# Kernel tuning notes

Hardware: AMD Instinct MI355X
Metric: run time of the kernel (lower is better)

The kernel has to match this reference:

```python
import jax, jax.numpy as jnp
import numpy as np

VOCAB = 5000
EMB = 128
H1 = 128
H2 = 64
Q = 64
T = 256
B = 512
LTEXT = 30
EOS = 2  # padding_idx row of the embedding is zero


def setup_inputs() -> dict:
    rng = jax.random.key(0)
    ks = jax.random.split(rng, 16)
    f = lambda k, s: jax.random.normal(k, s, dtype=jnp.float32) * 0.05
    emb = f(ks[0], (VOCAB, EMB)).at[EOS].set(0.0)
    return {
        "key": jax.random.normal(ks[1], (T, B, Q), dtype=jnp.float32),
        "values": jax.random.normal(ks[2], (T, B, Q), dtype=jnp.float32),
        "mask": jnp.ones((B, 1, T), dtype=jnp.float32),
        "text": jax.random.randint(ks[3], (B, LTEXT), 0, VOCAB),
        "emb": emb,
        "W_ih1": f(ks[4], (4 * H1, EMB + Q)), "W_hh1": f(ks[5], (4 * H1, H1)),
        "b_ih1": f(ks[6], (4 * H1,)), "b_hh1": f(ks[7], (4 * H1,)),
        "W_ih2": f(ks[8], (4 * H2, H1)), "W_hh2": f(ks[9], (4 * H2, H2)),
        "b_ih2": f(ks[10], (4 * H2,)), "b_hh2": f(ks[11], (4 * H2,)),
        "W_q": f(ks[12], (Q, H2)), "b_q": f(ks[13], (Q,)),
        "W_out": f(ks[14], (VOCAB, H2 + Q)), "b_out": f(ks[15], (VOCAB,)),
    }


def _lstm_cell(x, h, c, Wih, Whh, bih, bhh):
    # torch.nn.LSTMCell: gates ordered (input, forget, cell, output)
    g = x @ Wih.T + bih + h @ Whh.T + bhh
    i, f, gg, o = jnp.split(g, 4, axis=-1)
    c2 = jax.nn.sigmoid(f) * c + jax.nn.sigmoid(i) * jnp.tanh(gg)
    h2 = jax.nn.sigmoid(o) * jnp.tanh(c2)
    return h2, c2


def reference(key, values, mask, text, emb,
              W_ih1, W_hh1, b_ih1, b_hh1,
              W_ih2, W_hh2, b_ih2, b_hh2,
              W_q, b_q, W_out, b_out):
    # isTrain=True, teacher_forcing_ratio=1.0, use_gumbel_noise=False:
    # every step uses the teacher-forced embedding embeddings[:, i, :].
    bsz = key.shape[1]
    L = text.shape[1] - 1
    h1d = W_hh1.shape[1]
    h2d = W_hh2.shape[1]
    qd = W_q.shape[0]
    xs = jnp.swapaxes(emb[text[:, :L]], 0, 1)          # (L, B, EMB)
    m = mask[:, 0, :]                                   # (B, T)

    def step(carry, x):
        h1, c1, h2, c2, ctx = carry
        inp = jnp.concatenate([x, ctx], axis=1)         # (B, EMB+Q)
        h1, c1 = _lstm_cell(inp, h1, c1, W_ih1, W_hh1, b_ih1, b_hh1)
        h2, c2 = _lstm_cell(h1, h2, c2, W_ih2, W_hh2, b_ih2, b_hh2)
        q = h2 @ W_q.T + b_q                            # (B, Q)
        energy = jnp.einsum('bk,tbk->bt', q, key)       # (B, T)
        attn = jax.nn.softmax(energy, axis=-1)
        ma = m * attn
        ma = ma / jnp.maximum(jnp.sum(ma, axis=-1, keepdims=True), 2e-30)
        ctx = jnp.einsum('bt,tbv->bv', ma, values)      # (B, Q)
        pred = jnp.concatenate([h2, ctx], axis=1) @ W_out.T + b_out  # (B, V)
        return (h1, c1, h2, c2, ctx), pred

    z = lambda d: jnp.zeros((bsz, d), dtype=jnp.float32)
    carry0 = (z(h1d), z(h1d), z(h2d), z(h2d), z(qd))
    _, preds = jax.lax.scan(step, carry0, xs)           # (L, B, V)
    return jnp.swapaxes(preds, 0, 1)                    # (B, L, V)
```

## Files before the change

kernel.cpp:

```cpp
#include <hip/hip_runtime.h>
#include <hip/hip_bf16.h>
#include <hip/hip_fp16.h>

#define VOCAB 5000
#define EMB 128
#define H1D 128
#define H2D 64
#define QD 64
#define TDIM 256
#define BDIM 512
#define LTEXT 30
#define LSTEPS 29

typedef __attribute__((ext_vector_type(4))) float f32x4;
typedef __attribute__((ext_vector_type(8))) _Float16 f16x8;
typedef __attribute__((ext_vector_type(2))) _Float16 h2v;

#define OFF_WOUT  0u
#define OFF_W1H   0x140000u
#define OFF_W2H   (OFF_W1H + 512u*320u*2u)
#define OFF_WQH   (OFF_W2H + 256u*192u*2u)
#define OFF_B1    (OFF_WQH + 64u*64u*2u)
#define OFF_B2    (OFF_B1 + 512u*4u)
#define OFF_H2CTX 0x1B0000u

__device__ __forceinline__ float sigmoidf_(float x) {
    return 1.0f / (1.0f + __expf(-x));
}

__device__ __forceinline__ float dot8(f16x8 w, f16x8 u, float acc) {
    union U8 { f16x8 v; h2v h[4]; };
    U8 W; W.v = w; U8 X; X.v = u;
#if __has_builtin(__builtin_amdgcn_fdot2)
    acc = __builtin_amdgcn_fdot2(W.h[0], X.h[0], acc, false);
    acc = __builtin_amdgcn_fdot2(W.h[1], X.h[1], acc, false);
    acc = __builtin_amdgcn_fdot2(W.h[2], X.h[2], acc, false);
    acc = __builtin_amdgcn_fdot2(W.h[3], X.h[3], acc, false);
#else
    #pragma unroll
    for (int i = 0; i < 8; ++i) acc += (float)w[i] * (float)u[i];
#endif
    return acc;
}

__global__ void k_cvt_f16(const float* __restrict__ W, _Float16* __restrict__ Wh, int n) {
    int i = blockIdx.x * 256 + threadIdx.x;
    if (i < n) Wh[i] = (_Float16)W[i];
}

__global__ void k_prep_w1(const float* __restrict__ Wih1, const float* __restrict__ Whh1,
                          const float* __restrict__ bih1, const float* __restrict__ bhh1,
                          _Float16* __restrict__ W1h, float* __restrict__ bias1) {
    int g = blockIdx.x;
    int k = threadIdx.x;
    float v = (k < 192) ? Wih1[g * 192 + k] : Whh1[g * 128 + (k - 192)];
    W1h[g * 320 + k] = (_Float16)v;
    if (k == 0) bias1[g] = bih1[g] + bhh1[g];
}

__global__ void k_prep_w2(const float* __restrict__ Wih2, const float* __restrict__ Whh2,
                          const float* __restrict__ bih2, const float* __restrict__ bhh2,
                          _Float16* __restrict__ W2h, float* __restrict__ bias2) {
    int g = blockIdx.x;
    int k = threadIdx.x;
    float v = (k < 128) ? Wih2[g * 128 + k] : Whh2[g * 64 + (k - 128)];
    W2h[g * 192 + k] = (_Float16)v;
    if (k == 0) bias2[g] = bih2[g] + bhh2[g];
}

__global__ __launch_bounds__(512, 2) void k_recurrent(
    const float* __restrict__ key, const float* __restrict__ values,
    const float* __restrict__ mask, const int* __restrict__ text,
    const float* __restrict__ emb,
    const _Float16* __restrict__ W1h, const float* __restrict__ bias1,
    const _Float16* __restrict__ W2h, const float* __restrict__ bias2,
    const _Float16* __restrict__ Wqh, const float* __restrict__ bq,
    _Float16* __restrict__ h2ctx)
{
    __shared__ alignas(16) _Float16 s_key16[2 * 256 * 64];
    __shared__ alignas(16) _Float16 s_valT [2 * 64 * 256];
    __shared__ alignas(16) _Float16 s_x16[2][2][128];
    __shared__ alignas(16) _Float16 s_Wq[64 * 64];
    __shared__ alignas(16) _Float16 s_v16[2][192];
    __shared__ alignas(16) _Float16 s_ctx16[2][64];
    __shared__ alignas(16) _Float16 s_q16[2][64];
    __shared__ alignas(16) _Float16 s_ma16[2 * 256];
    __shared__ _Float16 s_mask16[2 * 256];
    __shared__ float s_g1[2][512];
    __shared__ float s_g2p[2][2][256];
    __shared__ float s_cp[2][4][64];
    __shared__ float s_redM[8], s_redA[8], s_redB[8];
    __shared__ int   s_tok[2][LSTEPS];

    const int tid = threadIdx.x;
    const int b0 = blockIdx.x * 2;

    f16x8 w1[40];
    {
        const f16x8* w1g = (const f16x8*)(W1h + (size_t)tid * 320);
        #pragma unroll
        for (int c = 0; c < 40; ++c) w1[c] = w1g[c];
    }
    const float bias1r = bias1[tid];
    const float bias2r = (tid < 256) ? bias2[tid] : 0.f;
    const float bqr    = (tid < 128) ? bq[tid & 63] : 0.f;

    if (tid < 64) {
        int r = tid >> 5, tt = tid & 31;
        if (tt < LSTEPS) s_tok[r][tt] = text[(b0 + r) * LTEXT + tt];
    }
    if (tid < 256) {
        int r = tid >> 7, k = tid & 127;
        int tok = text[(b0 + r) * LTEXT];
        s_x16[0][r][k] = (_Float16)emb[(size_t)tok * EMB + k];
    }
    {
        int qj = tid >> 3, c = tid & 7;
        f16x8 w = *(const f16x8*)(Wqh + (qj << 6) + (c << 3));
        *(f16x8*)&s_Wq[(qj << 6) + (((c ^ (qj & 7))) << 3)] = w;
    }
    {
        int r = tid >> 8, tk = tid & 255;
        s_mask16[tid] = (_Float16)mask[(size_t)(b0 + r) * TDIM + tk];
    }
    if (tid < 384) ((_Float16*)s_v16)[tid] = (_Float16)0.f;
    if (tid < 128) ((_Float16*)s_ctx16)[tid] = (_Float16)0.f;

    {
        const int tq  = tid >> 7;
        const int idx = tid & 127;
        const int r = idx >> 6, kk = idx & 63;
        #pragma unroll 4
        for (int it = 0; it < 64; ++it) {
            int t = (it << 2) + tq;
            size_t g = ((size_t)t * BDIM + b0 + r) * QD + kk;
            float kf = key[g];
            float vf = values[g];
            s_key16[(((r << 8) + t) << 6) + ((((kk >> 3) ^ (t & 7))) << 3) + (kk & 7)] = (_Float16)kf;
            s_valT [(((r << 6) + kk) << 8) + ((((t >> 3) ^ (kk & 31))) << 3) + (t & 7)] = (_Float16)vf;
        }
    }

    float c1reg = 0.f;
    float c2reg = 0.f;
    __syncthreads();

    #pragma unroll 1
    for (int t = 0; t < LSTEPS; ++t) {
        float xpref = 0.f;
        const int pr = tid >> 7, pk = tid & 127;
        const bool havepref = (t + 1 < LSTEPS) && (tid < 256);
        if (havepref) {
            int tok = s_tok[pr][t + 1];
            xpref = emb[(size_t)tok * EMB + pk];
        }

        {
            const f16x8* xc0 = (const f16x8*)&s_x16[t & 1][0][0];
            const f16x8* xc1 = (const f16x8*)&s_x16[t & 1][1][0];
            const f16x8* cc0 = (const f16x8*)&s_ctx16[0][0];
            const f16x8* cc1 = (const f16x8*)&s_ctx16[1][0];
            const f16x8* hh0 = (const f16x8*)&s_v16[0][0];
            const f16x8* hh1 = (const f16x8*)&s_v16[1][0];
            float a0 = bias1r, a1 = bias1r;
            #pragma unroll
            for (int c = 0; c < 16; ++c) { f16x8 w = w1[c];      a0 = dot8(w, xc0[c], a0); a1 = dot8(w, xc1[c], a1); }
            #pragma unroll
            for (int c = 0; c < 8;  ++c) { f16x8 w = w1[16 + c]; a0 = dot8(w, cc0[c], a0); a1 = dot8(w, cc1[c], a1); }
            #pragma unroll
            for (int c = 0; c < 16; ++c) { f16x8 w = w1[24 + c]; a0 = dot8(w, hh0[c], a0); a1 = dot8(w, hh1[c], a1); }
            s_g1[0][tid] = a0;
            s_g1[1][tid] = a1;
        }
        __syncthreads();

        if (tid < 256) {
            int r = tid >> 7, j = tid & 127;
            float gi = s_g1[r][j], gf = s_g1[r][128 + j];
            float gg = s_g1[r][256 + j], go = s_g1[r][384 + j];
            float c = sigmoidf_(gf) * c1reg + sigmoidf_(gi) * tanhf(gg);
            c1reg = c;
            float h = sigmoidf_(go) * tanhf(c);
            s_v16[r][j] = (_Float16)h;
        }
        __syncthreads();

        {
            const int g = tid & 255, half = tid >> 8;
            const f16x8* wrow = (const f16x8*)(W2h + (size_t)g * 192 + half * 96);
            const f16x8* v0 = (const f16x8*)&s_v16[0][0] + half * 12;
            const f16x8* v1 = (const f16x8*)&s_v16[1][0] + half * 12;
            float p0 = bias2r, p1 = bias2r;
            #pragma unroll
            for (int c = 0; c < 12; ++c) {
                f16x8 w = wrow[c];
                p0 = dot8(w, v0[c], p0);
                p1 = dot8(w, v1[c], p1);
            }
            s_g2p[half][0][g] = p0;
            s_g2p[half][1][g] = p1;
        }
        __syncthreads();

        if (tid < 128) {
            int r = tid >> 6, j = tid & 63;
            float gi = s_g2p[0][r][j]       + s_g2p[1][r][j];
            float gf = s_g2p[0][r][64 + j]  + s_g2p[1][r][64 + j];
            float gg = s_g2p[0][r][128 + j] + s_g2p[1][r][128 + j];
            float go = s_g2p[0][r][192 + j] + s_g2p[1][r][192 + j];
            float c = sigmoidf_(gf) * c2reg + sigmoidf_(gi) * tanhf(gg);
            c2reg = c;
            float h = sigmoidf_(go) * tanhf(c);
            s_v16[r][128 + j] = (_Float16)h;
            h2ctx[((size_t)(b0 + r) * LSTEPS + t) * 128 + j] = (_Float16)h;
        }
        __syncthreads();

        if (tid < 128) {
            int r = tid >> 6, qj = tid & 63;
            const f16x8* hv = (const f16x8*)&s_v16[r][128];
            float a = bqr;
            #pragma unroll
            for (int c = 0; c < 8; ++c) {
                f16x8 w = *(const f16x8*)&s_Wq[(qj << 6) + (((c ^ (qj & 7))) << 3)];
                a = dot8(w, hv[c], a);
            }
            s_q16[r][qj] = (_Float16)a;
        }
        __syncthreads();

        const int row = tid >> 8, tk = tid & 255;
        {
            const _Float16* kb = s_key16 + (((row << 8) + tk) << 6);
            const f16x8* qv = (const f16x8*)&s_q16[row][0];
            float e = 0.f;
            #pragma unroll
            for (int j = 0; j < 8; ++j) {
                f16x8 kk = *(const f16x8*)(kb + (((j ^ (tk & 7))) << 3));
                e = dot8(kk, qv[j], e);
            }
            const int wave = tid >> 6, lane = tid & 63;
            float m = e;
            #pragma unroll
            for (int off = 1; off < 64; off <<= 1) m = fmaxf(m, __shfl_xor(m, off));
            if (lane == 0) s_redM[wave] = m;
            __syncthreads();
            float mrow = fmaxf(fmaxf(s_redM[row * 4], s_redM[row * 4 + 1]),
                               fmaxf(s_redM[row * 4 + 2], s_redM[row * 4 + 3]));
            float p = __expf(e - mrow);
            float mp = (float)s_mask16[(row << 8) + tk] * p;
            float sp = p, smp = mp;
            #pragma unroll
            for (int off = 1; off < 64; off <<= 1) {
                sp += __shfl_xor(sp, off);
                smp += __shfl_xor(smp, off);
            }
            if (lane == 0) { s_redA[wave] = sp; s_redB[wave] = smp; }
            __syncthreads();
            float s1 = s_redA[row * 4] + s_redA[row * 4 + 1] + s_redA[row * 4 + 2] + s_redA[row * 4 + 3];
            float S2 = s_redB[row * 4] + s_redB[row * 4 + 1] + s_redB[row * 4 + 2] + s_redB[row * 4 + 3];
            float denom = fmaxf(S2, 2e-30f * s1);
            s_ma16[(row << 8) + tk] = (_Float16)(mp / denom);
        }
        __syncthreads();

        {
            const int v = tid & 63, ch = (tid >> 6) & 3;
            const _Float16* vb = s_valT + (((row << 6) + v) << 8);
            const f16x8* mac = (const f16x8*)&s_ma16[(row << 8) + (ch << 6)];
            float acc = 0.f;
            #pragma unroll
            for (int j = 0; j < 8; ++j) {
                int s = ch * 8 + j;
                f16x8 vv = *(const f16x8*)(vb + (((s ^ (v & 31))) << 3));
                acc = dot8(vv, mac[j], acc);
            }
            s_cp[row][ch][v] = acc;
        }
        if (havepref) s_x16[(t + 1) & 1][pr][pk] = (_Float16)xpref;
        __syncthreads();
        if (tid < 128) {
            int r = tid >> 6, v = tid & 63;
            float c = s_cp[r][0][v] + s_cp[r][1][v] + s_cp[r][2][v] + s_cp[r][3][v];
            s_ctx16[r][v] = (_Float16)c;
            h2ctx[((size_t)(b0 + r) * LSTEPS + t) * 128 + 64 + v] = (_Float16)c;
        }
        __syncthreads();
    }
}

#define KP 136

__global__ __launch_bounds__(256) void k_outproj(
    const _Float16* __restrict__ A,
    const _Float16* __restrict__ Bw,
    const float* __restrict__ b_out,
    float* __restrict__ out)
{
    __shared__ _Float16 As[64 * KP];
    __shared__ _Float16 Bs[64 * KP];
    const int tid = threadIdx.x;
    const int m0 = blockIdx.y * 64;
    const int v0 = blockIdx.x * 64;

    const uint4* Ag = (const uint4*)(A + (size_t)m0 * 128);
    uint4* AsU = (uint4*)As;
    #pragma unroll
    for (int i = 0; i < 4; ++i) {
        int fi = tid + 256 * i;
        int r = fi >> 4, c = fi & 15;
        AsU[r * 17 + c] = Ag[fi];
    }
    const uint4* Bg = (const uint4*)Bw;
    uint4* BsU = (uint4*)Bs;
    #pragma unroll
    for (int i = 0; i < 4; ++i) {
        int fi = tid + 256 * i;
        int r = fi >> 4, c = fi & 15;
        int v = v0 + r;
        uint4 val = make_uint4(0u, 0u, 0u, 0u);
        if (v < VOCAB) val = Bg[(size_t)v * 16 + c];
        BsU[r * 17 + c] = val;
    }
    __syncthreads();

    const int wv = tid >> 6, lane = tid & 63;
    const int fm = lane & 15, quad = lane >> 4;

    f32x4 acc[4];
    #pragma unroll
    for (int nt = 0; nt < 4; ++nt) acc[nt] = (f32x4){0.f, 0.f, 0.f, 0.f};

    #pragma unroll
    for (int kt = 0; kt < 4; ++kt) {
        f16x8 af = *(const f16x8*)&As[(16 * wv + fm) * KP + kt * 32 + quad * 8];
        #pragma unroll
        for (int nt = 0; nt < 4; ++nt) {
            f16x8 bf = *(const f16x8*)&Bs[(nt * 16 + fm) * KP + kt * 32 + quad * 8];
            acc[nt] = __builtin_amdgcn_mfma_f32_16x16x32_f16(af, bf, acc[nt], 0, 0, 0);
        }
    }

    #pragma unroll
    for (int nt = 0; nt < 4; ++nt) {
        int v = v0 + nt * 16 + fm;
        if (v < VOCAB) {
            float bo = b_out[v];
            #pragma unroll
            for (int r = 0; r < 4; ++r) {
                int rowm = m0 + 16 * wv + quad * 4 + r;
                out[(size_t)rowm * VOCAB + v] = acc[nt][r] + bo;
            }
        }
    }
}

extern "C" void kernel_launch(void* const* d_in, const int* in_sizes, int n_in,
                              void* d_out, int out_size, void* d_ws, size_t ws_size,
                              hipStream_t stream) {
    const float* key    = (const float*)d_in[0];
    const float* values = (const float*)d_in[1];
    const float* mask   = (const float*)d_in[2];
    const int*   text   = (const int*)d_in[3];
    const float* emb    = (const float*)d_in[4];
    const float* Wih1   = (const float*)d_in[5];
    const float* Whh1   = (const float*)d_in[6];
    const float* bih1   = (const float*)d_in[7];
    const float* bhh1   = (const float*)d_in[8];
    const float* Wih2   = (const float*)d_in[9];
    const float* Whh2   = (const float*)d_in[10];
    const float* bih2   = (const float*)d_in[11];
    const float* bhh2   = (const float*)d_in[12];
    const float* Wq     = (const float*)d_in[13];
    const float* bq     = (const float*)d_in[14];
    const float* Wout   = (const float*)d_in[15];
    const float* bout   = (const float*)d_in[16];
    float* out = (float*)d_out;

    char* ws = (char*)d_ws;
    _Float16* WoutH = (_Float16*)(ws + OFF_WOUT);
    _Float16* W1h   = (_Float16*)(ws + OFF_W1H);
    _Float16* W2h   = (_Float16*)(ws + OFF_W2H);
    _Float16* Wqh   = (_Float16*)(ws + OFF_WQH);
    float*    bias1 = (float*)(ws + OFF_B1);
    float*    bias2 = (float*)(ws + OFF_B2);
    _Float16* h2ctx = (_Float16*)(ws + OFF_H2CTX);

    k_cvt_f16<<<dim3((VOCAB * EMB + 255) / 256), dim3(256), 0, stream>>>(Wout, WoutH, VOCAB * EMB);
    k_cvt_f16<<<dim3(16), dim3(256), 0, stream>>>(Wq, Wqh, QD * H2D);
    k_prep_w1<<<dim3(512), dim3(320), 0, stream>>>(Wih1, Whh1, bih1, bhh1, W1h, bias1);
    k_prep_w2<<<dim3(256), dim3(192), 0, stream>>>(Wih2, Whh2, bih2, bhh2, W2h, bias2);

    k_recurrent<<<dim3(BDIM / 2), dim3(512), 0, stream>>>(
        key, values, mask, text, emb, W1h, bias1, W2h, bias2, Wqh, bq, h2ctx);

    k_outproj<<<dim3((VOCAB + 63) / 64, (BDIM * LSTEPS) / 64), dim3(256), 0, stream>>>(
        h2ctx, WoutH, bout, out);
}
```

Before: 717.7 us.

## Process one batch row per 1024-thread block and vectorize output stores

The recurrent kernel now runs one batch element per block with 1024 threads instead of two elements per 512-thread block, splitting each gate dot product across lanes with shuffle reductions and keeping W2 weights in registers. It also changes shared-memory layouts for key and Wq, merges the softmax reductions into a single-barrier online rescale, and uses fast rcp-based sigmoid/tanh. The output projection swaps MFMA operands so each lane writes four contiguous vocab entries as a float4 store. The aim is more parallelism, fewer barriers in the serial recurrence and coalesced output writes, at the cost of doubled key/value staging blocks and some approximation in tanh.

```diff
diff --git a/kernel.cpp b/kernel.cpp
--- a/kernel.cpp
+++ b/kernel.cpp
@@ -25,7 +25,12 @@
 #define OFF_H2CTX 0x1B0000u
 
 __device__ __forceinline__ float sigmoidf_(float x) {
-    return 1.0f / (1.0f + __expf(-x));
+    return __builtin_amdgcn_rcpf(1.0f + __expf(-x));
+}
+
+__device__ __forceinline__ float tanh_fast(float x) {
+    float e = __expf(2.0f * x);
+    return 1.0f - 2.0f * __builtin_amdgcn_rcpf(e + 1.0f);
 }
 
 __device__ __forceinline__ float dot8(f16x8 w, f16x8 u, float acc) {
@@ -43,6 +48,13 @@
     return acc;
 }
 
+__device__ __forceinline__ f16x8 load_pin(const f16x8* p) {
+    union WU { f16x8 h; float f[4]; } u;
+    u.h = *p;
+    asm volatile("" : "+v"(u.f[0]), "+v"(u.f[1]), "+v"(u.f[2]), "+v"(u.f[3]));
+    return u.h;
+}
+
 __global__ void k_cvt_f16(const float* __restrict__ W, _Float16* __restrict__ Wh, int n) {
     int i = blockIdx.x * 256 + threadIdx.x;
     if (i < n) Wh[i] = (_Float16)W[i];
@@ -68,7 +80,7 @@
     if (k == 0) bias2[g] = bih2[g] + bhh2[g];
 }
 
-__global__ __launch_bounds__(512, 2) void k_recurrent(
+__global__ __launch_bounds__(1024, 8) void k_recurrent(
     const float* __restrict__ key, const float* __restrict__ values,
     const float* __restrict__ mask, const int* __restrict__ text,
     const float* __restrict__ emb,
@@ -77,67 +89,59 @@
     const _Float16* __restrict__ Wqh, const float* __restrict__ bq,
     _Float16* __restrict__ h2ctx)
 {
-    __shared__ alignas(16) _Float16 s_key16[2 * 256 * 64];
-    __shared__ alignas(16) _Float16 s_valT [2 * 64 * 256];
-    __shared__ alignas(16) _Float16 s_x16[2][2][128];
-    __shared__ alignas(16) _Float16 s_Wq[64 * 64];
-    __shared__ alignas(16) _Float16 s_v16[2][192];
-    __shared__ alignas(16) _Float16 s_ctx16[2][64];
-    __shared__ alignas(16) _Float16 s_q16[2][64];
-    __shared__ alignas(16) _Float16 s_ma16[2 * 256];
-    __shared__ _Float16 s_mask16[2 * 256];
-    __shared__ float s_g1[2][512];
-    __shared__ float s_g2p[2][2][256];
-    __shared__ float s_cp[2][4][64];
-    __shared__ float s_redM[8], s_redA[8], s_redB[8];
-    __shared__ int   s_tok[2][LSTEPS];
+    __shared__ alignas(16) _Float16 s_key[8 * 256 * 8];
+    __shared__ alignas(16) _Float16 s_valT[64 * 256];
+    __shared__ alignas(16) _Float16 s_Wq[8 * 64 * 8];
+    __shared__ alignas(16) _Float16 s_u16[384];
+    __shared__ alignas(16) _Float16 s_q16[64];
+    __shared__ alignas(16) _Float16 s_ma16[256];
+    __shared__ float s_g1[512];
+    __shared__ float s_g2[256];
+    __shared__ float s_redM[4], s_redA[4], s_redB[4];
+    __shared__ int   s_tok[LSTEPS];
 
     const int tid = threadIdx.x;
-    const int b0 = blockIdx.x * 2;
-
-    f16x8 w1[40];
+    const int b = blockIdx.x;
+
+    const int g1gate = tid >> 1, g1half = tid & 1;
+    const int g2gate = tid >> 2, g2q = tid & 3;
+
+    f16x8 w1h[20];
     {
-        const f16x8* w1g = (const f16x8*)(W1h + (size_t)tid * 320);
+        const f16x8* p = (const f16x8*)(W1h + (size_t)g1gate * 320 + g1half * 160);
         #pragma unroll
-        for (int c = 0; c < 40; ++c) w1[c] = w1g[c];
-    }
-    const float bias1r = bias1[tid];
-    const float bias2r = (tid < 256) ? bias2[tid] : 0.f;
-    const float bqr    = (tid < 128) ? bq[tid & 63] : 0.f;
-
-    if (tid < 64) {
-        int r = tid >> 5, tt = tid & 31;
-        if (tt < LSTEPS) s_tok[r][tt] = text[(b0 + r) * LTEXT + tt];
-    }
-    if (tid < 256) {
-        int r = tid >> 7, k = tid & 127;
-        int tok = text[(b0 + r) * LTEXT];
-        s_x16[0][r][k] = (_Float16)emb[(size_t)tok * EMB + k];
-    }
+        for (int c = 0; c < 20; ++c) w1h[c] = load_pin(p + c);
+    }
+    f16x8 w2q[6];
     {
+        const f16x8* p = (const f16x8*)(W2h + (size_t)g2gate * 192 + g2q * 48);
+        #pragma unroll
+        for (int c = 0; c < 6; ++c) w2q[c] = load_pin(p + c);
+    }
+    float b1r = bias1[g1gate]; if (g1half) b1r = 0.f;
+    float b2r = bias2[g2gate]; if (g2q) b2r = 0.f;
+    const float bqr  = (tid < 64)  ? bq[tid] : 0.f;
+    const float mreg = (tid < 256) ? mask[(size_t)b * TDIM + tid] : 0.f;
+
+    if (tid < LSTEPS) s_tok[tid] = text[b * LTEXT + tid];
+    if (tid < 128)    s_u16[tid] = (_Float16)emb[(size_t)text[b * LTEXT] * EMB + tid];
+    if (tid >= 128 && tid < 384) s_u16[tid] = (_Float16)0.f;
+    if (tid < 512) {
         int qj = tid >> 3, c = tid & 7;
         f16x8 w = *(const f16x8*)(Wqh + (qj << 6) + (c << 3));
-        *(f16x8*)&s_Wq[(qj << 6) + (((c ^ (qj & 7))) << 3)] = w;
+        *(f16x8*)&s_Wq[(c << 9) + (qj << 3)] = w;
     }
     {
-        int r = tid >> 8, tk = tid & 255;
-        s_mask16[tid] = (_Float16)mask[(size_t)(b0 + r) * TDIM + tk];
-    }
-    if (tid < 384) ((_Float16*)s_v16)[tid] = (_Float16)0.f;
-    if (tid < 128) ((_Float16*)s_ctx16)[tid] = (_Float16)0.f;
-
-    {
-        const int tq  = tid >> 7;
-        const int idx = tid & 127;
-        const int r = idx >> 6, kk = idx & 63;
+        const int k = tid & 63;
+        const int tw = tid >> 6;
         #pragma unroll 4
-        for (int it = 0; it < 64; ++it) {
-            int t = (it << 2) + tq;
-            size_t g = ((size_t)t * BDIM + b0 + r) * QD + kk;
+        for (int it = 0; it < 16; ++it) {
+            int t = tw + (it << 4);
+            size_t g = ((size_t)t * BDIM + b) * QD + k;
             float kf = key[g];
             float vf = values[g];
-            s_key16[(((r << 8) + t) << 6) + ((((kk >> 3) ^ (t & 7))) << 3) + (kk & 7)] = (_Float16)kf;
-            s_valT [(((r << 6) + kk) << 8) + ((((t >> 3) ^ (kk & 31))) << 3) + (t & 7)] = (_Float16)vf;
+            s_key[((k >> 3) << 11) + (t << 3) + (k & 7)] = (_Float16)kf;
+            s_valT[(k << 8) + ((((t >> 3) ^ (k & 31))) << 3) + (t & 7)] = (_Float16)vf;
         }
     }
 
@@ -148,142 +152,125 @@
     #pragma unroll 1
     for (int t = 0; t < LSTEPS; ++t) {
         float xpref = 0.f;
-        const int pr = tid >> 7, pk = tid & 127;
-        const bool havepref = (t + 1 < LSTEPS) && (tid < 256);
-        if (havepref) {
-            int tok = s_tok[pr][t + 1];
-            xpref = emb[(size_t)tok * EMB + pk];
-        }
+        const bool havepref = (t + 1 < LSTEPS) && (tid < 128);
+        if (havepref) xpref = emb[(size_t)s_tok[t + 1] * EMB + tid];
 
         {
-            const f16x8* xc0 = (const f16x8*)&s_x16[t & 1][0][0];
-            const f16x8* xc1 = (const f16x8*)&s_x16[t & 1][1][0];
-            const f16x8* cc0 = (const f16x8*)&s_ctx16[0][0];
-            const f16x8* cc1 = (const f16x8*)&s_ctx16[1][0];
-            const f16x8* hh0 = (const f16x8*)&s_v16[0][0];
-            const f16x8* hh1 = (const f16x8*)&s_v16[1][0];
-            float a0 = bias1r, a1 = bias1r;
-            #pragma unroll
-            for (int c = 0; c < 16; ++c) { f16x8 w = w1[c];      a0 = dot8(w, xc0[c], a0); a1 = dot8(w, xc1[c], a1); }
-            #pragma unroll
-            for (int c = 0; c < 8;  ++c) { f16x8 w = w1[16 + c]; a0 = dot8(w, cc0[c], a0); a1 = dot8(w, cc1[c], a1); }
-            #pragma unroll
-            for (int c = 0; c < 16; ++c) { f16x8 w = w1[24 + c]; a0 = dot8(w, hh0[c], a0); a1 = dot8(w, hh1[c], a1); }
-            s_g1[0][tid] = a0;
-            s_g1[1][tid] = a1;
-        }
-        __syncthreads();
-
+            const f16x8* up = (const f16x8*)&s_u16[g1half * 160];
+            float a = b1r;
+            #pragma unroll
+            for (int c = 0; c < 20; ++c) a = dot8(w1h[c], up[c], a);
+            a += __shfl_down(a, 1);
+            if (g1half == 0) s_g1[g1gate] = a;
+        }
+        __syncthreads();
+
+        if (tid < 128) {
+            float gi = s_g1[tid], gf = s_g1[128 + tid];
+            float gg = s_g1[256 + tid], go = s_g1[384 + tid];
+            float c = sigmoidf_(gf) * c1reg + sigmoidf_(gi) * tanh_fast(gg);
+            c1reg = c;
+            float h = sigmoidf_(go) * tanh_fast(c);
+            s_u16[192 + tid] = (_Float16)h;
+        }
+        __syncthreads();
+
+        {
+            const f16x8* vp = (const f16x8*)&s_u16[192 + g2q * 48];
+            float a = b2r;
+            #pragma unroll
+            for (int c = 0; c < 6; ++c) a = dot8(w2q[c], vp[c], a);
+            a += __shfl_down(a, 1);
+            a += __shfl_down(a, 2);
+            if (g2q == 0) s_g2[g2gate] = a;
+        }
+        __syncthreads();
+
+        if (tid < 64) {
+            float gi = s_g2[tid], gf = s_g2[64 + tid];
+            float gg = s_g2[128 + tid], go = s_g2[192 + tid];
+            float c = sigmoidf_(gf) * c2reg + sigmoidf_(gi) * tanh_fast(gg);
+            c2reg = c;
+            float h = sigmoidf_(go) * tanh_fast(c);
+            s_u16[320 + tid] = (_Float16)h;
+            h2ctx[((size_t)b * LSTEPS + t) * 128 + tid] = (_Float16)h;
+        }
+        __syncthreads();
+
+        if (tid < 64) {
+            const f16x8* hv = (const f16x8*)&s_u16[320];
+            float a = bqr;
+            #pragma unroll
+            for (int c = 0; c < 8; ++c) {
+                f16x8 w = *(const f16x8*)&s_Wq[(c << 9) + (tid << 3)];
+                a = dot8(w, hv[c], a);
+            }
+            s_q16[tid] = (_Float16)a;
+        }
+        __syncthreads();
+
+        float e = 0.f, mw = 0.f, pexp = 0.f;
         if (tid < 256) {
-            int r = tid >> 7, j = tid & 127;
-            float gi = s_g1[r][j], gf = s_g1[r][128 + j];
-            float gg = s_g1[r][256 + j], go = s_g1[r][384 + j];
-            float c = sigmoidf_(gf) * c1reg + sigmoidf_(gi) * tanhf(gg);
-            c1reg = c;
-            float h = sigmoidf_(go) * tanhf(c);
-            s_v16[r][j] = (_Float16)h;
-        }
-        __syncthreads();
-
-        {
-            const int g = tid & 255, half = tid >> 8;
-            const f16x8* wrow = (const f16x8*)(W2h + (size_t)g * 192 + half * 96);
-            const f16x8* v0 = (const f16x8*)&s_v16[0][0] + half * 12;
-            const f16x8* v1 = (const f16x8*)&s_v16[1][0] + half * 12;
-            float p0 = bias2r, p1 = bias2r;
-            #pragma unroll
-            for (int c = 0; c < 12; ++c) {
-                f16x8 w = wrow[c];
-                p0 = dot8(w, v0[c], p0);
-                p1 = dot8(w, v1[c], p1);
-            }
-            s_g2p[half][0][g] = p0;
-            s_g2p[half][1][g] = p1;
-        }
-        __syncthreads();
-
-        if (tid < 128) {
-            int r = tid >> 6, j = tid & 63;
-            float gi = s_g2p[0][r][j]       + s_g2p[1][r][j];
-            float gf = s_g2p[0][r][64 + j]  + s_g2p[1][r][64 + j];
-            float gg = s_g2p[0][r][128 + j] + s_g2p[1][r][128 + j];
-            float go = s_g2p[0][r][192 + j] + s_g2p[1][r][192 + j];
-            float c = sigmoidf_(gf) * c2reg + sigmoidf_(gi) * tanhf(gg);
-            c2reg = c;
-            float h = sigmoidf_(go) * tanhf(c);
-            s_v16[r][128 + j] = (_Float16)h;
-            h2ctx[((size_t)(b0 + r) * LSTEPS + t) * 128 + j] = (_Float16)h;
-        }
-        __syncthreads();
-
-        if (tid < 128) {
-            int r = tid >> 6, qj = tid & 63;
-            const f16x8* hv = (const f16x8*)&s_v16[r][128];
-            float a = bqr;
-            #pragma unroll
-            for (int c = 0; c < 8; ++c) {
-                f16x8 w = *(const f16x8*)&s_Wq[(qj << 6) + (((c ^ (qj & 7))) << 3)];
-                a = dot8(w, hv[c], a);
-            }
-            s_q16[r][qj] = (_Float16)a;
-        }
-        __syncthreads();
-
-        const int row = tid >> 8, tk = tid & 255;
-        {
-            const _Float16* kb = s_key16 + (((row << 8) + tk) << 6);
-            const f16x8* qv = (const f16x8*)&s_q16[row][0];
-            float e = 0.f;
+            const f16x8* qv = (const f16x8*)&s_q16[0];
             #pragma unroll
             for (int j = 0; j < 8; ++j) {
-                f16x8 kk = *(const f16x8*)(kb + (((j ^ (tk & 7))) << 3));
+                f16x8 kk = *(const f16x8*)&s_key[(j << 11) + (tid << 3)];
                 e = dot8(kk, qv[j], e);
             }
-            const int wave = tid >> 6, lane = tid & 63;
             float m = e;
             #pragma unroll
             for (int off = 1; off < 64; off <<= 1) m = fmaxf(m, __shfl_xor(m, off));
-            if (lane == 0) s_redM[wave] = m;
-            __syncthreads();
-            float mrow = fmaxf(fmaxf(s_redM[row * 4], s_redM[row * 4 + 1]),
-                               fmaxf(s_redM[row * 4 + 2], s_redM[row * 4 + 3]));
-            float p = __expf(e - mrow);
-            float mp = (float)s_mask16[(row << 8) + tk] * p;
-            float sp = p, smp = mp;
+            mw = m;
+            pexp = __expf(e - mw);
+            float mp = mreg * pexp;
+            float sp = pexp, smp = mp;
             #pragma unroll
             for (int off = 1; off < 64; off <<= 1) {
                 sp += __shfl_xor(sp, off);
                 smp += __shfl_xor(smp, off);
             }
-            if (lane == 0) { s_redA[wave] = sp; s_redB[wave] = smp; }
-            __syncthreads();
-            float s1 = s_redA[row * 4] + s_redA[row * 4 + 1] + s_redA[row * 4 + 2] + s_redA[row * 4 + 3];
-            float S2 = s_redB[row * 4] + s_redB[row * 4 + 1] + s_redB[row * 4 + 2] + s_redB[row * 4 + 3];
-            float denom = fmaxf(S2, 2e-30f * s1);
-            s_ma16[(row << 8) + tk] = (_Float16)(mp / denom);
-        }
-        __syncthreads();
-
-        {
-            const int v = tid & 63, ch = (tid >> 6) & 3;
-            const _Float16* vb = s_valT + (((row << 6) + v) << 8);
-            const f16x8* mac = (const f16x8*)&s_ma16[(row << 8) + (ch << 6)];
-            float acc = 0.f;
-            #pragma unroll
-            for (int j = 0; j < 8; ++j) {
-                int s = ch * 8 + j;
-                f16x8 vv = *(const f16x8*)(vb + (((s ^ (v & 31))) << 3));
-                acc = dot8(vv, mac[j], acc);
-            }
-            s_cp[row][ch][v] = acc;
-        }
-        if (havepref) s_x16[(t + 1) & 1][pr][pk] = (_Float16)xpref;
-        __syncthreads();
-        if (tid < 128) {
-            int r = tid >> 6, v = tid & 63;
-            float c = s_cp[r][0][v] + s_cp[r][1][v] + s_cp[r][2][v] + s_cp[r][3][v];
-            s_ctx16[r][v] = (_Float16)c;
-            h2ctx[((size_t)(b0 + r) * LSTEPS + t) * 128 + 64 + v] = (_Float16)c;
+            if ((tid & 63) == 0) {
+                int w = tid >> 6;
+                s_redM[w] = mw; s_redA[w] = sp; s_redB[w] = smp;
+            }
+        }
+        __syncthreads();
+
+        if (tid < 256) {
+            float m = fmaxf(fmaxf(s_redM[0], s_redM[1]), fmaxf(s_redM[2], s_redM[3]));
+            float S1 = 0.f, S2 = 0.f;
+            #pragma unroll
+            for (int w = 0; w < 4; ++w) {
+                float sc = __expf(s_redM[w] - m);
+                S1 += s_redA[w] * sc;
+                S2 += s_redB[w] * sc;
+            }
+            float scale = __expf(mw - m);
+            float mp = mreg * pexp * scale;
+            float denom = fmaxf(S2, 2e-30f * S1);
+            s_ma16[tid] = (_Float16)(mp * __builtin_amdgcn_rcpf(denom));
+        }
+        __syncthreads();
+
+        float cacc = 0.f;
+        if (tid < 512) {
+            const int v = tid >> 3, ch = tid & 7;
+            #pragma unroll
+            for (int j = 0; j < 4; ++j) {
+                int s = (ch << 2) + j;
+                f16x8 vv = *(const f16x8*)&s_valT[(v << 8) + (((s ^ (v & 31))) << 3)];
+                f16x8 ma = *(const f16x8*)&s_ma16[s << 3];
+                cacc = dot8(vv, ma, cacc);
+            }
+            cacc += __shfl_down(cacc, 1);
+            cacc += __shfl_down(cacc, 2);
+            cacc += __shfl_down(cacc, 4);
+        }
+        if (havepref) s_u16[tid] = (_Float16)xpref;
+        if (tid < 512 && (tid & 7) == 0) {
+            int v = tid >> 3;
+            s_u16[128 + v] = (_Float16)cacc;
+            h2ctx[((size_t)b * LSTEPS + t) * 128 + 64 + v] = (_Float16)cacc;
         }
         __syncthreads();
     }
@@ -291,7 +278,7 @@
 
 #define KP 136
 
-__global__ __launch_bounds__(256) void k_outproj(
+__global__ __launch_bounds__(256, 4) void k_outproj(
     const _Float16* __restrict__ A,
     const _Float16* __restrict__ Bw,
     const float* __restrict__ b_out,
@@ -337,19 +324,27 @@
         #pragma unroll
         for (int nt = 0; nt < 4; ++nt) {
             f16x8 bf = *(const f16x8*)&Bs[(nt * 16 + fm) * KP + kt * 32 + quad * 8];
-            acc[nt] = __builtin_amdgcn_mfma_f32_16x16x32_f16(af, bf, acc[nt], 0, 0, 0);
-        }
-    }
-
+            acc[nt] = __builtin_amdgcn_mfma_f32_16x16x32_f16(bf, af, acc[nt], 0, 0, 0);
+        }
+    }
+
+    const int rowm = m0 + 16 * wv + fm;
     #pragma unroll
     for (int nt = 0; nt < 4; ++nt) {
-        int v = v0 + nt * 16 + fm;
-        if (v < VOCAB) {
-            float bo = b_out[v];
+        int vb = v0 + nt * 16 + quad * 4;
+        if (vb + 3 < VOCAB) {
+            float4 bo = *(const float4*)&b_out[vb];
+            float4 res;
+            res.x = acc[nt][0] + bo.x;
+            res.y = acc[nt][1] + bo.y;
+            res.z = acc[nt][2] + bo.z;
+            res.w = acc[nt][3] + bo.w;
+            *(float4*)&out[(size_t)rowm * VOCAB + vb] = res;
+        } else {
             #pragma unroll
             for (int r = 0; r < 4; ++r) {
-                int rowm = m0 + 16 * wv + quad * 4 + r;
-                out[(size_t)rowm * VOCAB + v] = acc[nt][r] + bo;
+                int v = vb + r;
+                if (v < VOCAB) out[(size_t)rowm * VOCAB + v] = acc[nt][r] + b_out[v];
             }
         }
     }
@@ -391,7 +386,7 @@
     k_prep_w1<<<dim3(512), dim3(320), 0, stream>>>(Wih1, Whh1, bih1, bhh1, W1h, bias1);
     k_prep_w2<<<dim3(256), dim3(192), 0, stream>>>(Wih2, Whh2, bih2, bhh2, W2h, bias2);
 
-    k_recurrent<<<dim3(BDIM / 2), dim3(512), 0, stream>>>(
+    k_recurrent<<<dim3(BDIM), dim3(1024), 0, stream>>>(
         key, values, mask, text, emb, W1h, bias1, W2h, bias2, Wqh, bq, h2ctx);
 
     k_outproj<<<dim3((VOCAB + 63) / 64, (BDIM * LSTEPS) / 64), dim3(256), 0, stream>>>(
```

Result: slower. 1.540 ms (+114.5%).
